# Kernel tuning notes

Hardware: AMD Instinct MI355X
Metric: run time of the kernel (lower is better)

## Reference

```python
import jax, jax.numpy as jnp
import numpy as np

B, L, S, DIM, H, DH, DFF = 2, 2048, 2048, 1024, 16, 64, 4096
EPS = 1e-6


def _ln(x, w, b):
    m = jnp.mean(x, axis=-1, keepdims=True)
    v = jnp.mean(jnp.square(x - m), axis=-1, keepdims=True)
    return (x - m) / jnp.sqrt(v + EPS) * w + b


def _mha(q, k, v, mask):
    # q: [B,L,H*DH], k/v: [B,S,H*DH], mask broadcastable to [B,H,L,S], True = masked
    b, l, _ = q.shape
    s = k.shape[1]
    q = q.reshape(b, l, H, DH)
    k = k.reshape(b, s, H, DH)
    v = v.reshape(b, s, H, DH)
    scale = 1.0 / np.sqrt(DH).astype(np.float32)
    attn = jnp.einsum('blhd,bshd->bhls', q, k) * scale
    if mask is not None:
        attn = jnp.where(mask, -jnp.inf, attn)
    attn = jax.nn.softmax(attn, axis=-1)
    out = jnp.einsum('bhls,bshd->blhd', attn, v)
    return out.reshape(b, l, H * DH)


def setup_inputs() -> dict:
    key = jax.random.key(0)
    ks = jax.random.split(key, 12)
    std = 0.02
    inp = {
        'input': jax.random.normal(ks[0], (B, L, DIM), jnp.float32),
        'source': jax.random.normal(ks[1], (B, S, DIM), jnp.float32),
        # source mask: no source positions masked
        'source_mask': jnp.zeros((B, 1, 1, S), bool),
        # causal mask for self-attention (True above diagonal -> masked)
        'mask': jnp.triu(jnp.ones((L, L), bool), 1)[None, None],
        # self-attention
        'ln_self_w': jnp.ones((DIM,), jnp.float32),
        'ln_self_b': jnp.zeros((DIM,), jnp.float32),
        'w_qkv': std * jax.random.normal(ks[2], (DIM, 3 * DIM), jnp.float32),
        'b_qkv': jnp.zeros((3 * DIM,), jnp.float32),
        'w_so': std * jax.random.normal(ks[3], (DIM, DIM), jnp.float32),
        'b_so': jnp.zeros((DIM,), jnp.float32),
        # cross-attention
        'ln_cross_w': jnp.ones((DIM,), jnp.float32),
        'ln_cross_b': jnp.zeros((DIM,), jnp.float32),
        'w_q': std * jax.random.normal(ks[4], (DIM, DIM), jnp.float32),
        'b_q': jnp.zeros((DIM,), jnp.float32),
        'w_kv': std * jax.random.normal(ks[5], (DIM, 2 * DIM), jnp.float32),
        'b_kv': jnp.zeros((2 * DIM,), jnp.float32),
        'w_co': std * jax.random.normal(ks[6], (DIM, DIM), jnp.float32),
        'b_co': jnp.zeros((DIM,), jnp.float32),
        # MLP (1 layer)
        'ln_mlp_w': jnp.ones((DIM,), jnp.float32),
        'ln_mlp_b': jnp.zeros((DIM,), jnp.float32),
        'w_ff1': std * jax.random.normal(ks[7], (DIM, DFF), jnp.float32),
        'b_ff1': jnp.zeros((DFF,), jnp.float32),
        'w_ff2': std * jax.random.normal(ks[8], (DFF, DIM), jnp.float32),
        'b_ff2': jnp.zeros((DIM,), jnp.float32),
    }
    return inp


def reference(input, source, source_mask, mask,
              ln_self_w, ln_self_b, w_qkv, b_qkv, w_so, b_so,
              ln_cross_w, ln_cross_b, w_q, b_q, w_kv, b_kv, w_co, b_co,
              ln_mlp_w, ln_mlp_b, w_ff1, b_ff1, w_ff2, b_ff2):
    x = input
    # self-attention block (pre-LN)
    h = _ln(x, ln_self_w, ln_self_b)
    qkv = h @ w_qkv + b_qkv
    q, k, v = jnp.split(qkv, 3, axis=-1)
    sa = _mha(q, k, v, mask) @ w_so + b_so
    x = x + sa
    # cross-attention block (pre-LN)
    h = _ln(x, ln_cross_w, ln_cross_b)
    q = h @ w_q + b_q
    kv = source @ w_kv + b_kv
    k, v = jnp.split(kv, 2, axis=-1)
    ca = _mha(q, k, v, source_mask) @ w_co + b_co
    x = x + ca
    # feed-forward block (pre-LN), eval mode (no dropout/droppath)
    h = _ln(x, ln_mlp_w, ln_mlp_b)
    ff = jax.nn.gelu(h @ w_ff1 + b_ff1, approximate=False) @ w_ff2 + b_ff2
    x = x + ff
    return x
```

## Files before the change

### kernel.cpp

```cpp
#include <hip/hip_runtime.h>
#include <hip/hip_bf16.h>
#include <math.h>

typedef __bf16 bf16_t;
typedef __bf16 bf16x8 __attribute__((ext_vector_type(8)));
typedef __bf16 bf16x4 __attribute__((ext_vector_type(4)));
typedef float  f32x4  __attribute__((ext_vector_type(4)));

#define DIM   1024
#define NB    2
#define NL    2048
#define NS    2048
#define NH    16
#define NDH   64
#define NDFF  4096

__device__ __forceinline__ bf16x8 ld_bf16x8(const bf16_t* p) {
    return *reinterpret_cast<const bf16x8*>(p);
}

__device__ __forceinline__ void gl_lds16(const bf16_t* g, bf16_t* l) {
    __builtin_amdgcn_global_load_lds(
        (const __attribute__((address_space(1))) void*)g,
        (__attribute__((address_space(3))) void*)l, 16, 0, 0);
}

__global__ __launch_bounds__(256)
void wconv_kernel(const float* __restrict__ in, bf16_t* __restrict__ out, int K, int N)
{
    __shared__ float tile[32][33];
    int n0 = blockIdx.x * 32, k0 = blockIdx.y * 32;
    int tx = threadIdx.x & 31, ty = threadIdx.x >> 5;
    #pragma unroll
    for (int j = 0; j < 4; ++j)
        tile[ty + 8*j][tx] = in[(size_t)(k0 + ty + 8*j) * N + n0 + tx];
    __syncthreads();
    #pragma unroll
    for (int j = 0; j < 4; ++j)
        out[(size_t)(n0 + ty + 8*j) * K + k0 + tx] = (bf16_t)tile[tx][ty + 8*j];
}

__global__ __launch_bounds__(256)
void f2b_kernel(const float* __restrict__ in, bf16_t* __restrict__ out)
{
    size_t i = ((size_t)blockIdx.x * 256 + threadIdx.x) * 4;
    float4 v = *reinterpret_cast<const float4*>(in + i);
    bf16x4 o = { (bf16_t)v.x, (bf16_t)v.y, (bf16_t)v.z, (bf16_t)v.w };
    *reinterpret_cast<bf16x4*>(out + i) = o;
}

__global__ __launch_bounds__(256)
void ln_kernel(const float* __restrict__ x, const float* __restrict__ wgt,
               const float* __restrict__ bia, bf16_t* __restrict__ out)
{
    int row = blockIdx.x, tid = threadIdx.x;
    float4 xv = reinterpret_cast<const float4*>(x + (size_t)row * DIM)[tid];
    float s1 = xv.x + xv.y + xv.z + xv.w;
    float s2 = xv.x*xv.x + xv.y*xv.y + xv.z*xv.z + xv.w*xv.w;
    #pragma unroll
    for (int off = 32; off > 0; off >>= 1) {
        s1 += __shfl_xor(s1, off, 64);
        s2 += __shfl_xor(s2, off, 64);
    }
    __shared__ float red[8];
    int w = tid >> 6;
    if ((tid & 63) == 0) { red[w] = s1; red[w + 4] = s2; }
    __syncthreads();
    s1 = red[0] + red[1] + red[2] + red[3];
    s2 = red[4] + red[5] + red[6] + red[7];
    float mean = s1 * (1.0f / DIM);
    float var  = s2 * (1.0f / DIM) - mean * mean;
    float rstd = rsqrtf(var + 1e-6f);
    float4 wv = reinterpret_cast<const float4*>(wgt)[tid];
    float4 bv = reinterpret_cast<const float4*>(bia)[tid];
    bf16x4 o = { (bf16_t)((xv.x - mean) * rstd * wv.x + bv.x),
                 (bf16_t)((xv.y - mean) * rstd * wv.y + bv.y),
                 (bf16_t)((xv.z - mean) * rstd * wv.z + bv.z),
                 (bf16_t)((xv.w - mean) * rstd * wv.w + bv.w) };
    reinterpret_cast<bf16x4*>(out + (size_t)row * DIM)[tid] = o;
}

template<int EPI, int BM, int BN>
__global__ __launch_bounds__(256)
void gemm_kernel(const bf16_t* __restrict__ A, const bf16_t* __restrict__ BT,
                 const float* __restrict__ bias, const float* __restrict__ res,
                 void* __restrict__ out, int M, int N, int K)
{
    constexpr int WM = BM / 2, WN = BN / 2;
    constexpr int AM = WM / 16, AN = WN / 16;
    constexpr int ABE = (BM + BN) * 32;
    constexpr int LPS = (BM + BN) / 64;
    __shared__ __align__(16) bf16_t lds[3 * ABE];

    int tid = threadIdx.x;
    int lane = tid & 63, w = tid >> 6;
    int wr = w >> 1, wc = w & 1;
    int la = lane & 15, lg = lane >> 4;
    int m0 = blockIdx.y * BM, n0 = blockIdx.x * BN;

    f32x4 acc[AM][AN] = {};

    int sr = lane >> 2;
    int sc = ((lane & 3) ^ (sr & 3)) * 8;
    const bf16_t* Ap = A  + (size_t)(m0 + w * (BM / 4) + sr) * K + sc;
    const bf16_t* Bp = BT + (size_t)(n0 + w * (BN / 4) + sr) * K + sc;

    auto stage = [&](int t, int buf) {
        int k0 = t * 32;
        bf16_t* base = &lds[buf * ABE];
        #pragma unroll
        for (int i = 0; i < BM / 64; ++i)
            gl_lds16(Ap + ((size_t)i * 16) * K + k0, base + (w * (BM / 4) + i * 16) * 32);
        #pragma unroll
        for (int i = 0; i < BN / 64; ++i)
            gl_lds16(Bp + ((size_t)i * 16) * K + k0, base + (BM + w * (BN / 4) + i * 16) * 32);
    };

    auto compute = [&](int buf) {
        const bf16_t* base = &lds[buf * ABE];
        int cs = (lg ^ (la & 3)) * 8;
        bf16x8 af[AM], bfr[AN];
        #pragma unroll
        for (int mi = 0; mi < AM; ++mi)
            af[mi] = ld_bf16x8(base + (wr * WM + mi * 16 + la) * 32 + cs);
        #pragma unroll
        for (int ni = 0; ni < AN; ++ni)
            bfr[ni] = ld_bf16x8(base + (BM + wc * WN + ni * 16 + la) * 32 + cs);
        #pragma unroll
        for (int mi = 0; mi < AM; ++mi)
            #pragma unroll
            for (int ni = 0; ni < AN; ++ni)
                acc[mi][ni] = __builtin_amdgcn_mfma_f32_16x16x32_bf16(
                                  af[mi], bfr[ni], acc[mi][ni], 0, 0, 0);
    };

    int nt = K / 32;
    stage(0, 0);
    stage(1, 1);
    int buf = 0;
    for (int t = 0; t < nt - 1; ++t) {
        asm volatile("s_waitcnt vmcnt(%0)" :: "n"(LPS) : "memory");
        __builtin_amdgcn_s_barrier();
        __builtin_amdgcn_sched_barrier(0);
        if (t + 2 < nt) stage(t + 2, (t + 2) % 3);
        compute(buf);
        buf = (buf == 2) ? 0 : buf + 1;
    }
    asm volatile("s_waitcnt vmcnt(0)" ::: "memory");
    __builtin_amdgcn_s_barrier();
    __builtin_amdgcn_sched_barrier(0);
    compute(buf);

    #pragma unroll
    for (int mi = 0; mi < AM; ++mi) {
        #pragma unroll
        for (int ni = 0; ni < AN; ++ni) {
            #pragma unroll
            for (int i = 0; i < 4; ++i) {
                int row = m0 + wr * WM + mi * 16 + lg * 4 + i;
                int col = n0 + wc * WN + ni * 16 + la;
                float v = acc[mi][ni][i] + bias[col];
                if (EPI == 1) v = 0.5f * v * (1.0f + erff(v * 0.70710678118f));
                if (EPI == 2)
                    ((float*)out)[(size_t)row * N + col] = res[(size_t)row * N + col] + v;
                else
                    ((bf16_t*)out)[(size_t)row * N + col] = (bf16_t)v;
            }
        }
    }
}

template<int EPI>
__global__ __launch_bounds__(512, 2)
void gemm256_kernel(const bf16_t* __restrict__ A, const bf16_t* __restrict__ BT,
                    const float* __restrict__ bias, void* __restrict__ out,
                    int M, int N, int K, int nbx)
{
    constexpr int BM = 256, BN = 256, BK = 32;
    constexpr int ABE = (BM + BN) * BK;
    __shared__ __align__(16) bf16_t lds[4 * ABE];

    int tid = threadIdx.x;
    int lane = tid & 63, w = tid >> 6;
    int wr = w >> 2, wc = w & 3;
    int la = lane & 15, lg = lane >> 4;

    int nwg = gridDim.x, bid = blockIdx.x;
    int swz = (bid & 7) * (nwg >> 3) + (bid >> 3);
    int m0 = (swz / nbx) * BM, n0 = (swz % nbx) * BN;

    f32x4 acc[8][4] = {};

    int sr = tid >> 2;
    int sc = ((tid & 3) ^ (sr & 3)) * 8;
    const bf16_t* Ap = A  + (size_t)(m0 + sr) * K + sc;
    const bf16_t* Bp = BT + (size_t)(n0 + sr) * K + sc;

    auto stage = [&](int t, int buf) {
        int k0 = t * BK;
        bf16_t* base = &lds[buf * ABE];
        #pragma unroll
        for (int i = 0; i < 2; ++i)
            gl_lds16(Ap + (size_t)(i * 128) * K + k0, base + (i * 128 + w * 16) * BK);
        #pragma unroll
        for (int i = 0; i < 2; ++i)
            gl_lds16(Bp + (size_t)(i * 128) * K + k0, base + BM * BK + (i * 128 + w * 16) * BK);
    };

    auto compute = [&](int buf) {
        const bf16_t* base = &lds[buf * ABE];
        int cs = (lg ^ (la & 3)) * 8;
        bf16x8 af[8], bfr[4];
        #pragma unroll
        for (int mi = 0; mi < 8; ++mi)
            af[mi] = ld_bf16x8(base + (wr * 128 + mi * 16 + la) * BK + cs);
        #pragma unroll
        for (int ni = 0; ni < 4; ++ni)
            bfr[ni] = ld_bf16x8(base + BM * BK + (wc * 64 + ni * 16 + la) * BK + cs);
        __builtin_amdgcn_s_setprio(1);
        #pragma unroll
        for (int mi = 0; mi < 8; ++mi)
            #pragma unroll
            for (int ni = 0; ni < 4; ++ni)
                acc[mi][ni] = __builtin_amdgcn_mfma_f32_16x16x32_bf16(
                                  af[mi], bfr[ni], acc[mi][ni], 0, 0, 0);
        __builtin_amdgcn_s_setprio(0);
    };

    int nt = K / BK;
    stage(0, 0); stage(1, 1); stage(2, 2);
    for (int t = 0; t < nt - 1; ++t) {
        asm volatile("s_waitcnt vmcnt(8)" ::: "memory");
        __builtin_amdgcn_s_barrier();
        __builtin_amdgcn_sched_barrier(0);
        if (t + 3 < nt) stage(t + 3, (t + 3) & 3);
        compute(t & 3);
    }
    asm volatile("s_waitcnt vmcnt(0)" ::: "memory");
    __builtin_amdgcn_s_barrier();
    __builtin_amdgcn_sched_barrier(0);
    compute((nt - 1) & 3);

    #pragma unroll
    for (int mi = 0; mi < 8; ++mi) {
        #pragma unroll
        for (int ni = 0; ni < 4; ++ni) {
            #pragma unroll
            for (int i = 0; i < 4; ++i) {
                int row = m0 + wr * 128 + mi * 16 + lg * 4 + i;
                int col = n0 + wc * 64 + ni * 16 + la;
                float v = acc[mi][ni][i] + bias[col];
                if (EPI == 1) v = 0.5f * v * (1.0f + erff(v * 0.70710678118f));
                ((bf16_t*)out)[(size_t)row * N + col] = (bf16_t)v;
            }
        }
    }
}

template<bool CAUSAL>
__global__ __launch_bounds__(256)
void attn_kernel(const bf16_t* __restrict__ Q, int qs,
                 const bf16_t* __restrict__ Kp, int ks,
                 const bf16_t* __restrict__ Vp, int vs,
                 bf16_t* __restrict__ O, int os, int L, int S)
{
    __shared__ __align__(16) bf16_t Ks[64 * 64];
    __shared__ __align__(16) bf16_t Vt[64 * 64];
    __shared__ __align__(16) bf16_t Ps[4][16 * 64];

    int tid = threadIdx.x, lane = tid & 63, w = tid >> 6;
    int la = lane & 15, lg = lane >> 4;
    int qtile = (CAUSAL ? (gridDim.x - 1 - blockIdx.x) : blockIdx.x) * 64;
    int b = blockIdx.y >> 4, h = blockIdx.y & 15;

    const bf16_t* qb = Q  + (size_t)(b * L) * qs + h * 64;
    const bf16_t* kb = Kp + (size_t)(b * S) * ks + h * 64;
    const bf16_t* vb = Vp + (size_t)(b * S) * vs + h * 64;
    bf16_t*       ob = O  + (size_t)(b * L) * os + h * 64;

    int qrow = qtile + w * 16 + la;
    bf16x8 qf0 = ld_bf16x8(qb + (size_t)qrow * qs + lg * 8);
    bf16x8 qf1 = ld_bf16x8(qb + (size_t)qrow * qs + 32 + lg * 8);
    #pragma unroll
    for (int j = 0; j < 8; ++j) { qf0[j] = qf0[j] * (bf16_t)0.125f; qf1[j] = qf1[j] * (bf16_t)0.125f; }

    f32x4 zero = {0.f, 0.f, 0.f, 0.f};
    f32x4 o[4];
    #pragma unroll
    for (int dt = 0; dt < 4; ++dt) o[dt] = zero;
    float lpart[4] = {0.f, 0.f, 0.f, 0.f};

    int rk  = tid >> 3;
    int ck8 = tid & 7;
    int sv0   = tid & 31;
    int dbase = (tid >> 5) * 8;
    int r7 = la & 7;

    int n_full = (CAUSAL ? qtile : S) / 64;
    int nit = n_full + (CAUSAL ? 1 : 0);

    bf16x8 kr0 = ld_bf16x8(kb + (size_t)rk * ks + ck8 * 8);
    bf16x8 kr1 = ld_bf16x8(kb + (size_t)(rk + 32) * ks + ck8 * 8);
    bf16x8 vr0 = ld_bf16x8(vb + (size_t)sv0 * vs + dbase);
    bf16x8 vr1 = ld_bf16x8(vb + (size_t)(sv0 + 32) * vs + dbase);

    for (int it = 0; it < nit; ++it) {
        int s0 = it * 64;
        bool diag = CAUSAL && (it == n_full);

        __syncthreads();
        *reinterpret_cast<bf16x8*>(&Ks[rk * 64 + ((ck8 ^ (rk & 7)) * 8)]) = kr0;
        *reinterpret_cast<bf16x8*>(&Ks[(rk + 32) * 64 + ((ck8 ^ (rk & 7)) * 8)]) = kr1;
        #pragma unroll
        for (int j = 0; j < 8; ++j) {
            Vt[(dbase + j) * 64 + (sv0 ^ (j << 3))]        = vr0[j];
            Vt[(dbase + j) * 64 + ((sv0 + 32) ^ (j << 3))] = vr1[j];
        }
        __syncthreads();

        if (it + 1 < nit) {
            int s1 = s0 + 64;
            kr0 = ld_bf16x8(kb + (size_t)(s1 + rk) * ks + ck8 * 8);
            kr1 = ld_bf16x8(kb + (size_t)(s1 + rk + 32) * ks + ck8 * 8);
            vr0 = ld_bf16x8(vb + (size_t)(s1 + sv0) * vs + dbase);
            vr1 = ld_bf16x8(vb + (size_t)(s1 + sv0 + 32) * vs + dbase);
        }

        f32x4 sf[4];
        #pragma unroll
        for (int ct = 0; ct < 4; ++ct) {
            const bf16_t* kr = &Ks[(ct * 16 + la) * 64];
            bf16x8 k0 = ld_bf16x8(kr + ((lg ^ r7) * 8));
            bf16x8 k1 = ld_bf16x8(kr + (((4 + lg) ^ r7) * 8));
            f32x4 z = zero;
            z = __builtin_amdgcn_mfma_f32_16x16x32_bf16(qf0, k0, z, 0, 0, 0);
            z = __builtin_amdgcn_mfma_f32_16x16x32_bf16(qf1, k1, z, 0, 0, 0);
            sf[ct] = z;
        }

        #pragma unroll
        for (int ct = 0; ct < 4; ++ct) {
            #pragma unroll
            for (int i = 0; i < 4; ++i) {
                float p = __expf(sf[ct][i]);
                if (diag) {
                    int sg = s0 + ct * 16 + la;
                    int qg = qtile + w * 16 + lg * 4 + i;
                    if (sg > qg) p = 0.f;
                }
                lpart[i] += p;
                int row = lg * 4 + i;
                Ps[w][row * 64 + ((ct * 16 + la) ^ ((row & 7) << 3))] = (bf16_t)p;
            }
        }

        bf16x8 pa0 = ld_bf16x8(&Ps[w][la * 64 + ((lg ^ r7) * 8)]);
        bf16x8 pa1 = ld_bf16x8(&Ps[w][la * 64 + (((4 + lg) ^ r7) * 8)]);
        #pragma unroll
        for (int dt = 0; dt < 4; ++dt) {
            const bf16_t* vr = &Vt[(dt * 16 + la) * 64];
            bf16x8 v0 = ld_bf16x8(vr + ((lg ^ r7) * 8));
            bf16x8 v1 = ld_bf16x8(vr + (((4 + lg) ^ r7) * 8));
            o[dt] = __builtin_amdgcn_mfma_f32_16x16x32_bf16(pa0, v0, o[dt], 0, 0, 0);
            o[dt] = __builtin_amdgcn_mfma_f32_16x16x32_bf16(pa1, v1, o[dt], 0, 0, 0);
        }
    }

    #pragma unroll
    for (int off = 1; off < 16; off <<= 1)
        #pragma unroll
        for (int i = 0; i < 4; ++i)
            lpart[i] += __shfl_xor(lpart[i], off, 64);

    #pragma unroll
    for (int dt = 0; dt < 4; ++dt)
        #pragma unroll
        for (int i = 0; i < 4; ++i) {
            int row = qtile + w * 16 + lg * 4 + i;
            float val = o[dt][i] / lpart[i];
            ob[(size_t)row * os + dt * 16 + la] = (bf16_t)val;
        }
}

extern "C" void kernel_launch(void* const* d_in, const int* in_sizes, int n_in,
                              void* d_out, int out_size, void* d_ws, size_t ws_size,
                              hipStream_t stream)
{
    const float* input     = (const float*)d_in[0];
    const float* source    = (const float*)d_in[1];
    const float* ln_self_w = (const float*)d_in[4];
    const float* ln_self_b = (const float*)d_in[5];
    const float* w_qkv     = (const float*)d_in[6];
    const float* b_qkv     = (const float*)d_in[7];
    const float* w_so      = (const float*)d_in[8];
    const float* b_so      = (const float*)d_in[9];
    const float* ln_cross_w= (const float*)d_in[10];
    const float* ln_cross_b= (const float*)d_in[11];
    const float* w_q       = (const float*)d_in[12];
    const float* b_q       = (const float*)d_in[13];
    const float* w_kv      = (const float*)d_in[14];
    const float* b_kv      = (const float*)d_in[15];
    const float* w_co      = (const float*)d_in[16];
    const float* b_co      = (const float*)d_in[17];
    const float* ln_mlp_w  = (const float*)d_in[18];
    const float* ln_mlp_b  = (const float*)d_in[19];
    const float* w_ff1     = (const float*)d_in[20];
    const float* b_ff1     = (const float*)d_in[21];
    const float* w_ff2     = (const float*)d_in[22];
    const float* b_ff2     = (const float*)d_in[23];

    const int M = NB * NL;

    char* ws = (char*)d_ws;
    size_t off = 0;
    auto alloc = [&](size_t bytes) { char* p = ws + off; off += (bytes + 255) & ~(size_t)255; return p; };

    bf16_t* wT_qkv = (bf16_t*)alloc((size_t)3072 * 1024 * 2);
    bf16_t* wT_so  = (bf16_t*)alloc((size_t)1024 * 1024 * 2);
    bf16_t* wT_q   = (bf16_t*)alloc((size_t)1024 * 1024 * 2);
    bf16_t* wT_kv  = (bf16_t*)alloc((size_t)2048 * 1024 * 2);
    bf16_t* wT_co  = (bf16_t*)alloc((size_t)1024 * 1024 * 2);
    bf16_t* wT_ff1 = (bf16_t*)alloc((size_t)4096 * 1024 * 2);
    bf16_t* wT_ff2 = (bf16_t*)alloc((size_t)1024 * 4096 * 2);
    bf16_t* srcb   = (bf16_t*)alloc((size_t)M * 1024 * 2);
    bf16_t* hbuf   = (bf16_t*)alloc((size_t)M * 1024 * 2);
    bf16_t* qkvb   = (bf16_t*)alloc((size_t)M * 3072 * 2);
    bf16_t* attnb  = (bf16_t*)alloc((size_t)M * 1024 * 2);
    bf16_t* qcb    = (bf16_t*)alloc((size_t)M * 1024 * 2);
    bf16_t* kvcb   = (bf16_t*)alloc((size_t)M * 2048 * 2);
    float*  xbuf   = (float*) alloc((size_t)M * 1024 * 4);
    bf16_t* ff1b   = (bf16_t*)alloc((size_t)M * 4096 * 2);
    (void)ws_size; (void)n_in; (void)in_sizes; (void)out_size;

    wconv_kernel<<<dim3(3072/32, 1024/32), 256, 0, stream>>>(w_qkv, wT_qkv, 1024, 3072);
    wconv_kernel<<<dim3(1024/32, 1024/32), 256, 0, stream>>>(w_so,  wT_so,  1024, 1024);
    wconv_kernel<<<dim3(1024/32, 1024/32), 256, 0, stream>>>(w_q,   wT_q,   1024, 1024);
    wconv_kernel<<<dim3(2048/32, 1024/32), 256, 0, stream>>>(w_kv,  wT_kv,  1024, 2048);
    wconv_kernel<<<dim3(1024/32, 1024/32), 256, 0, stream>>>(w_co,  wT_co,  1024, 1024);
    wconv_kernel<<<dim3(4096/32, 1024/32), 256, 0, stream>>>(w_ff1, wT_ff1, 1024, 4096);
    wconv_kernel<<<dim3(1024/32, 4096/32), 256, 0, stream>>>(w_ff2, wT_ff2, 4096, 1024);
    f2b_kernel<<<(M * 1024) / (256 * 4), 256, 0, stream>>>(source, srcb);

    ln_kernel<<<M, 256, 0, stream>>>(input, ln_self_w, ln_self_b, hbuf);
    gemm256_kernel<0><<<dim3((3072/256) * (M/256)), 512, 0, stream>>>(hbuf, wT_qkv, b_qkv, qkvb, M, 3072, 1024, 3072/256);
    attn_kernel<true><<<dim3(NL/64, NB*NH), 256, 0, stream>>>(qkvb, 3072, qkvb + 1024, 3072, qkvb + 2048, 3072,
                                                              attnb, 1024, NL, NL);
    gemm_kernel<2,128,64><<<dim3(1024/64, M/128), 256, 0, stream>>>(attnb, wT_so, b_so, input, xbuf, M, 1024, 1024);

    ln_kernel<<<M, 256, 0, stream>>>(xbuf, ln_cross_w, ln_cross_b, hbuf);
    gemm_kernel<0,128,64><<<dim3(1024/64, M/128), 256, 0, stream>>>(hbuf, wT_q, b_q, nullptr, qcb, M, 1024, 1024);
    gemm256_kernel<0><<<dim3((2048/256) * (M/256)), 512, 0, stream>>>(srcb, wT_kv, b_kv, kvcb, M, 2048, 1024, 2048/256);
    attn_kernel<false><<<dim3(NL/64, NB*NH), 256, 0, stream>>>(qcb, 1024, kvcb, 2048, kvcb + 1024, 2048,
                                                               attnb, 1024, NL, NS);
    gemm_kernel<2,128,64><<<dim3(1024/64, M/128), 256, 0, stream>>>(attnb, wT_co, b_co, xbuf, xbuf, M, 1024, 1024);

    ln_kernel<<<M, 256, 0, stream>>>(xbuf, ln_mlp_w, ln_mlp_b, hbuf);
    gemm256_kernel<1><<<dim3((4096/256) * (M/256)), 512, 0, stream>>>(hbuf, wT_ff1, b_ff1, ff1b, M, 4096, 1024, 4096/256);
    gemm_kernel<2,128,64><<<dim3(1024/64, M/128), 256, 0, stream>>>(ff1b, wT_ff2, b_ff2, xbuf, d_out, M, 1024, 4096);
}
```

Before: 477.7 us.

## Restructure GEMM LDS layout, use inline ds_read, retile QKV and KV GEMMs

Changes the LDS swizzle so the XOR uses bits 3-4 of the lane, and replaces the compiler LDS loads with inline-asm ds_read_b128 followed by an explicit lgkmcnt fence and priority boost around the MFMAs. The 256x256 GEMM is rewritten as gemm256d with a per-warp staging layout and a software-pipelined k-loop that issues the prefetch before the wait. Each k-tile is split into two MFMA halves to reduce register pressure, and the epilogue tiles get explicit vmcnt counts. The QKV and cross-KV projections move from the 256x256 kernel to the 128x128 gemm_kernel, giving more workgroups at the cost of less reuse per block; the explicit fences may also serialise LDS reads and MFMAs.

```diff
diff --git a/kernel.cpp b/kernel.cpp
--- a/kernel.cpp
+++ b/kernel.cpp
@@ -15,6 +15,14 @@
 #define NDH   64
 #define NDFF  4096
 
+template<int N> struct IC { static constexpr int value = N; };
+
+#define DS_READ_B128(dst, addr) \
+    asm volatile("ds_read_b128 %0, %1" : "=v"(dst) : "v"(addr))
+#define LGKM0_FENCE() do { \
+    asm volatile("s_waitcnt lgkmcnt(0)" ::: "memory"); \
+    __builtin_amdgcn_sched_barrier(0); } while (0)
+
 __device__ __forceinline__ bf16x8 ld_bf16x8(const bf16_t* p) {
     return *reinterpret_cast<const bf16x8*>(p);
 }
@@ -23,6 +31,10 @@
     __builtin_amdgcn_global_load_lds(
         (const __attribute__((address_space(1))) void*)g,
         (__attribute__((address_space(3))) void*)l, 16, 0, 0);
+}
+
+__device__ __forceinline__ unsigned lds_u32(const bf16_t* p) {
+    return (unsigned)(uintptr_t)(__attribute__((address_space(3))) const void*)p;
 }
 
 __global__ __launch_bounds__(256)
@@ -101,7 +113,7 @@
     f32x4 acc[AM][AN] = {};
 
     int sr = lane >> 2;
-    int sc = ((lane & 3) ^ (sr & 3)) * 8;
+    int sc = ((lane & 3) ^ ((lane >> 3) & 3)) * 8;
     const bf16_t* Ap = A  + (size_t)(m0 + w * (BM / 4) + sr) * K + sc;
     const bf16_t* Bp = BT + (size_t)(n0 + w * (BN / 4) + sr) * K + sc;
 
@@ -116,22 +128,29 @@
             gl_lds16(Bp + ((size_t)i * 16) * K + k0, base + (BM + w * (BN / 4) + i * 16) * 32);
     };
 
+    unsigned ldsb = lds_u32(lds);
+    unsigned kla = (la >> 1) & 3;
+    unsigned a_base = ldsb + ((wr * WM + la) * 32 + (lg ^ kla) * 8) * 2;
+    unsigned b_base = ldsb + (BM * 32 + (wc * WN + la) * 32 + (lg ^ kla) * 8) * 2;
+
     auto compute = [&](int buf) {
-        const bf16_t* base = &lds[buf * ABE];
-        int cs = (lg ^ (la & 3)) * 8;
+        unsigned dB = (unsigned)(buf * ABE * 2);
         bf16x8 af[AM], bfr[AN];
         #pragma unroll
         for (int mi = 0; mi < AM; ++mi)
-            af[mi] = ld_bf16x8(base + (wr * WM + mi * 16 + la) * 32 + cs);
+            DS_READ_B128(af[mi], a_base + dB + mi * 1024);
         #pragma unroll
         for (int ni = 0; ni < AN; ++ni)
-            bfr[ni] = ld_bf16x8(base + (BM + wc * WN + ni * 16 + la) * 32 + cs);
+            DS_READ_B128(bfr[ni], b_base + dB + ni * 1024);
+        LGKM0_FENCE();
+        __builtin_amdgcn_s_setprio(1);
         #pragma unroll
         for (int mi = 0; mi < AM; ++mi)
             #pragma unroll
             for (int ni = 0; ni < AN; ++ni)
                 acc[mi][ni] = __builtin_amdgcn_mfma_f32_16x16x32_bf16(
                                   af[mi], bfr[ni], acc[mi][ni], 0, 0, 0);
+        __builtin_amdgcn_s_setprio(0);
     };
 
     int nt = K / 32;
@@ -172,13 +191,12 @@
 
 template<int EPI>
 __global__ __launch_bounds__(512, 2)
-void gemm256_kernel(const bf16_t* __restrict__ A, const bf16_t* __restrict__ BT,
-                    const float* __restrict__ bias, void* __restrict__ out,
-                    int M, int N, int K, int nbx)
-{
-    constexpr int BM = 256, BN = 256, BK = 32;
-    constexpr int ABE = (BM + BN) * BK;
-    __shared__ __align__(16) bf16_t lds[4 * ABE];
+void gemm256d_kernel(const bf16_t* __restrict__ A, const bf16_t* __restrict__ BT,
+                     const float* __restrict__ bias, void* __restrict__ out,
+                     int M, int N, int K, int nbx)
+{
+    constexpr int DBE = 16384;
+    __shared__ __align__(16) bf16_t lds[4 * DBE];
 
     int tid = threadIdx.x;
     int lane = tid & 63, w = tid >> 6;
@@ -187,59 +205,74 @@
 
     int nwg = gridDim.x, bid = blockIdx.x;
     int swz = (bid & 7) * (nwg >> 3) + (bid >> 3);
-    int m0 = (swz / nbx) * BM, n0 = (swz % nbx) * BN;
+    int m0 = (swz / nbx) * 256, n0 = (swz % nbx) * 256;
 
     f32x4 acc[8][4] = {};
 
-    int sr = tid >> 2;
-    int sc = ((tid & 3) ^ (sr & 3)) * 8;
-    const bf16_t* Ap = A  + (size_t)(m0 + sr) * K + sc;
-    const bf16_t* Bp = BT + (size_t)(n0 + sr) * K + sc;
-
-    auto stage = [&](int t, int buf) {
-        int k0 = t * BK;
-        bf16_t* base = &lds[buf * ABE];
-        #pragma unroll
-        for (int i = 0; i < 2; ++i)
-            gl_lds16(Ap + (size_t)(i * 128) * K + k0, base + (i * 128 + w * 16) * BK);
-        #pragma unroll
-        for (int i = 0; i < 2; ++i)
-            gl_lds16(Bp + (size_t)(i * 128) * K + k0, base + BM * BK + (i * 128 + w * 16) * BK);
+    int sr = lane >> 2;
+    int sc = ((lane & 3) ^ ((lane >> 3) & 3)) * 8;
+    const bf16_t* Ap = A  + (size_t)(m0 + w * 16 + sr) * K + sc;
+    const bf16_t* Bp = BT + (size_t)(n0 + w * 16 + sr) * K + sc;
+
+    auto stage = [&](int t) {
+        int k0 = t * 32;
+        bf16_t* base = &lds[(t & 3) * DBE];
+        gl_lds16(Ap + k0,                     base + w * 512);
+        gl_lds16(Ap + (size_t)128 * K + k0,   base + 4096 + w * 512);
+        gl_lds16(Bp + k0,                     base + 8192 + w * 512);
+        gl_lds16(Bp + (size_t)128 * K + k0,   base + 12288 + w * 512);
     };
 
-    auto compute = [&](int buf) {
-        const bf16_t* base = &lds[buf * ABE];
-        int cs = (lg ^ (la & 3)) * 8;
-        bf16x8 af[8], bfr[4];
-        #pragma unroll
-        for (int mi = 0; mi < 8; ++mi)
-            af[mi] = ld_bf16x8(base + (wr * 128 + mi * 16 + la) * BK + cs);
+    unsigned ldsb = lds_u32(lds);
+    unsigned kla = (la >> 1) & 3;
+    unsigned a_base = ldsb + ((wr * 128 + la) * 32 + (lg ^ kla) * 8) * 2;
+    unsigned b_base = ldsb + (8192 + (wc * 64 + la) * 32 + (lg ^ kla) * 8) * 2;
+
+    int nt = K / 32;
+
+    auto ktile = [&](int kt, auto vmc, bool do_stage) {
+        if (do_stage) stage(kt + 3);
+        asm volatile("s_waitcnt vmcnt(%0)" :: "n"(decltype(vmc)::value) : "memory");
+        __builtin_amdgcn_s_barrier();
+        __builtin_amdgcn_sched_barrier(0);
+        unsigned dB = (unsigned)((kt & 3) * (DBE * 2));
+        bf16x8 af[4], af2[4], bfr[4];
+        #pragma unroll
+        for (int mi = 0; mi < 4; ++mi)
+            DS_READ_B128(af[mi], a_base + dB + mi * 1024);
         #pragma unroll
         for (int ni = 0; ni < 4; ++ni)
-            bfr[ni] = ld_bf16x8(base + BM * BK + (wc * 64 + ni * 16 + la) * BK + cs);
+            DS_READ_B128(bfr[ni], b_base + dB + ni * 1024);
+        LGKM0_FENCE();
         __builtin_amdgcn_s_setprio(1);
         #pragma unroll
-        for (int mi = 0; mi < 8; ++mi)
+        for (int mi = 0; mi < 4; ++mi)
             #pragma unroll
             for (int ni = 0; ni < 4; ++ni)
                 acc[mi][ni] = __builtin_amdgcn_mfma_f32_16x16x32_bf16(
                                   af[mi], bfr[ni], acc[mi][ni], 0, 0, 0);
         __builtin_amdgcn_s_setprio(0);
-    };
-
-    int nt = K / BK;
-    stage(0, 0); stage(1, 1); stage(2, 2);
-    for (int t = 0; t < nt - 1; ++t) {
-        asm volatile("s_waitcnt vmcnt(8)" ::: "memory");
+        #pragma unroll
+        for (int mi = 0; mi < 4; ++mi)
+            DS_READ_B128(af2[mi], a_base + dB + (4 + mi) * 1024);
+        LGKM0_FENCE();
+        __builtin_amdgcn_s_setprio(1);
+        #pragma unroll
+        for (int mi = 0; mi < 4; ++mi)
+            #pragma unroll
+            for (int ni = 0; ni < 4; ++ni)
+                acc[4 + mi][ni] = __builtin_amdgcn_mfma_f32_16x16x32_bf16(
+                                      af2[mi], bfr[ni], acc[4 + mi][ni], 0, 0, 0);
+        __builtin_amdgcn_s_setprio(0);
         __builtin_amdgcn_s_barrier();
         __builtin_amdgcn_sched_barrier(0);
-        if (t + 3 < nt) stage(t + 3, (t + 3) & 3);
-        compute(t & 3);
-    }
-    asm volatile("s_waitcnt vmcnt(0)" ::: "memory");
-    __builtin_amdgcn_s_barrier();
-    __builtin_amdgcn_sched_barrier(0);
-    compute((nt - 1) & 3);
+    };
+
+    stage(0); stage(1); stage(2);
+    for (int kt = 0; kt < nt - 3; ++kt) ktile(kt, IC<12>{}, true);
+    ktile(nt - 3, IC<8>{}, false);
+    ktile(nt - 2, IC<4>{}, false);
+    ktile(nt - 1, IC<0>{}, false);
 
     #pragma unroll
     for (int mi = 0; mi < 8; ++mi) {
@@ -442,19 +475,19 @@
     f2b_kernel<<<(M * 1024) / (256 * 4), 256, 0, stream>>>(source, srcb);
 
     ln_kernel<<<M, 256, 0, stream>>>(input, ln_self_w, ln_self_b, hbuf);
-    gemm256_kernel<0><<<dim3((3072/256) * (M/256)), 512, 0, stream>>>(hbuf, wT_qkv, b_qkv, qkvb, M, 3072, 1024, 3072/256);
+    gemm_kernel<0,128,128><<<dim3(3072/128, M/128), 256, 0, stream>>>(hbuf, wT_qkv, b_qkv, nullptr, qkvb, M, 3072, 1024);
     attn_kernel<true><<<dim3(NL/64, NB*NH), 256, 0, stream>>>(qkvb, 3072, qkvb + 1024, 3072, qkvb + 2048, 3072,
                                                               attnb, 1024, NL, NL);
     gemm_kernel<2,128,64><<<dim3(1024/64, M/128), 256, 0, stream>>>(attnb, wT_so, b_so, input, xbuf, M, 1024, 1024);
 
     ln_kernel<<<M, 256, 0, stream>>>(xbuf, ln_cross_w, ln_cross_b, hbuf);
     gemm_kernel<0,128,64><<<dim3(1024/64, M/128), 256, 0, stream>>>(hbuf, wT_q, b_q, nullptr, qcb, M, 1024, 1024);
-    gemm256_kernel<0><<<dim3((2048/256) * (M/256)), 512, 0, stream>>>(srcb, wT_kv, b_kv, kvcb, M, 2048, 1024, 2048/256);
+    gemm_kernel<0,128,128><<<dim3(2048/128, M/128), 256, 0, stream>>>(srcb, wT_kv, b_kv, nullptr, kvcb, M, 2048, 1024);
     attn_kernel<false><<<dim3(NL/64, NB*NH), 256, 0, stream>>>(qcb, 1024, kvcb, 2048, kvcb + 1024, 2048,
                                                                attnb, 1024, NL, NS);
     gemm_kernel<2,128,64><<<dim3(1024/64, M/128), 256, 0, stream>>>(attnb, wT_co, b_co, xbuf, xbuf, M, 1024, 1024);
 
     ln_kernel<<<M, 256, 0, stream>>>(xbuf, ln_mlp_w, ln_mlp_b, hbuf);
-    gemm256_kernel<1><<<dim3((4096/256) * (M/256)), 512, 0, stream>>>(hbuf, wT_ff1, b_ff1, ff1b, M, 4096, 1024, 4096/256);
+    gemm256d_kernel<1><<<dim3((4096/256) * (M/256)), 512, 0, stream>>>(hbuf, wT_ff1, b_ff1, ff1b, M, 4096, 1024, 4096/256);
     gemm_kernel<2,128,64><<<dim3(1024/64, M/128), 256, 0, stream>>>(ff1b, wT_ff2, b_ff2, xbuf, d_out, M, 1024, 4096);
 }
```

Result: faster. 467.9 us (-2.0%).
